# Performance work log

Hardware: AMD Instinct MI355X
Metric: run time of the kernel (lower is better)

Reference implementation:

```python
import jax, jax.numpy as jnp
import numpy as np

T, B, DIM = 64, 16, 512
H, Dh, ETA = 8, 64, 4
FD = ETA * Dh  # feature_dim = 256
EPS = 1e-6


def setup_inputs() -> dict:
    key = jax.random.key(0)
    ks = jax.random.split(key, 12)

    def w(k, o, i):
        return jax.random.normal(k, (o, i), jnp.float32) * (1.0 / np.sqrt(i).astype(np.float32))

    return {
        "inputs": jax.random.normal(ks[0], (T, B, DIM), jnp.float32),
        "terminations": jax.random.randint(ks[1], (T, B), 0, 2).astype(jnp.int32),
        "kv_state_prev": jnp.zeros((B, H, FD, Dh), jnp.float32),
        "norm_state_prev": jnp.zeros((B, H, FD), jnp.float32),
        "Wq": w(ks[2], H * Dh, DIM),
        "Wk": w(ks[3], H * Dh, DIM),
        "Wv": w(ks[4], H * Dh, DIM),
        "Wb": w(ks[5], H * Dh, DIM),
        "Wg": w(ks[6], H * Dh, DIM),
        "Wp1": w(ks[7], H * ETA, DIM),
        "Wp2": w(ks[8], H * ETA, DIM),
        "Wp3": w(ks[9], H * ETA, DIM),
        "Wo": w(ks[10], DIM, H * Dh),
        "bo": jnp.zeros((DIM,), jnp.float32),
    }


def reference(inputs, terminations, kv_state_prev, norm_state_prev,
              Wq, Wk, Wv, Wb, Wg, Wp1, Wp2, Wp3, Wo, bo):
    def proj(W, e):
        return (inputs @ W.T).reshape(T, B, H, e)

    q = proj(Wq, Dh)
    k = proj(Wk, Dh)
    v = proj(Wv, Dh)
    beta = jax.nn.sigmoid(proj(Wb, Dh))
    gamma = jax.nn.sigmoid(proj(Wg, Dh))
    p1 = proj(Wp1, ETA)
    p2 = proj(Wp2, ETA)
    p3 = proj(Wp3, ETA)

    # feature map: outer product of relu(p) [eta] and x [head_dim] -> [eta*head_dim]
    def fmap(x, p):
        return jnp.einsum('tbhe,tbhd->tbhed', jax.nn.relu(p), x).reshape(T, B, H, FD)

    phi_q = fmap(q, p2)
    psi_k = fmap(k, p1)
    # gamma map: outer product of sigmoid(p3) and sigmoid-gated gamma, values in (0,1)
    gamma_feat = jnp.einsum('tbhe,tbhd->tbhed', jax.nn.sigmoid(p3), gamma).reshape(T, B, H, FD)

    gated_v = v * beta                       # [T,B,H,Dh]
    gated_k = psi_k * gamma_feat             # [T,B,H,FD]

    term_mask = (1.0 - terminations.astype(jnp.float32))[:, :, None, None]  # [T,B,1,1]
    discount = (1.0 - gamma_feat) * term_mask  # [T,B,H,FD]

    kv_upd = jnp.einsum('tbhd,tbhD->tbhDd', gated_v, gated_k)  # [T,B,H,FD,Dh]

    def step(carry, x):
        kv, nm = carry
        d, u_kv, u_nm = x
        kv = d[..., None] * kv + u_kv
        nm = d * nm + u_nm
        return (kv, nm), (kv, nm)

    _, (kv_all, nm_all) = jax.lax.scan(step, (kv_state_prev, norm_state_prev),
                                       (discount, kv_upd, gated_k))

    attn_num = jnp.einsum('tbhDd,tbhD->tbhd', kv_all, phi_q)
    attn_den = jnp.einsum('tbhD,tbhD->tbh', phi_q, nm_all)
    attn_out = (attn_num / (attn_den[..., None] + EPS)).reshape(T, B, H * Dh)
    output = attn_out @ Wo.T + bo
    return (output, kv_all[-1], nm_all[-1])
```

## Files before the change

### kernel.cpp

```cpp
#include <hip/hip_runtime.h>


#define T_N   64
#define B_N   16
#define DIM_N 512
#define H_N   8
#define DH_N  64

#define OUT_ELEMS   524288
#define KV_ELEMS    2097152
#define PROJ_ELEMS  2719744

typedef _Float16 f16;
typedef f16   f16x8 __attribute__((ext_vector_type(8)));
typedef float f32x4 __attribute__((ext_vector_type(4)));

__device__ __forceinline__ float sigmoidf_(float x) {
    return 1.0f / (1.0f + __expf(-x));
}

__device__ __forceinline__ void gemm64_core(const float* __restrict__ A,
                                            const float* __restrict__ W,
                                            const float* __restrict__ bias,
                                            float* __restrict__ C, int N,
                                            int mb, int nb, int kBase, int kLen) {
    const int nbase = nb * 64;
    if (nbase >= N) return;

    __shared__ float As[2][16][68];
    __shared__ float Bs[2][16][68];

    const int tid = threadIdx.x;
    const int mbase = mb * 64;
    const int tx = tid & 15;
    const int ty = tid >> 4;
    const int sr = tid >> 2;
    const int sk = (tid & 3) << 2;
    const bool wok = (nbase + sr) < N;

    const float* Ap = A + (size_t)(mbase + sr) * 512 + kBase + sk;
    const float* Wp = W + (size_t)(nbase + sr) * 512 + kBase + sk;

    float4 av = *(const float4*)Ap;
    float4 wv = wok ? *(const float4*)Wp : make_float4(0.f, 0.f, 0.f, 0.f);
    As[0][sk + 0][sr] = av.x; As[0][sk + 1][sr] = av.y;
    As[0][sk + 2][sr] = av.z; As[0][sk + 3][sr] = av.w;
    Bs[0][sk + 0][sr] = wv.x; Bs[0][sk + 1][sr] = wv.y;
    Bs[0][sk + 2][sr] = wv.z; Bs[0][sk + 3][sr] = wv.w;

    float acc[4][4];
    #pragma unroll
    for (int i = 0; i < 4; ++i)
        #pragma unroll
        for (int j = 0; j < 4; ++j) acc[i][j] = 0.f;

    for (int k0 = 0; k0 < kLen; k0 += 16) {
        const int buf = (k0 >> 4) & 1;
        __syncthreads();
        const bool more = (k0 + 16) < kLen;
        if (more) {
            av = *(const float4*)(Ap + k0 + 16);
            wv = wok ? *(const float4*)(Wp + k0 + 16) : make_float4(0.f, 0.f, 0.f, 0.f);
        }
        #pragma unroll
        for (int k = 0; k < 16; ++k) {
            float4 a  = *(const float4*)&As[buf][k][ty << 2];
            float4 bq = *(const float4*)&Bs[buf][k][tx << 2];
            float ar[4] = {a.x, a.y, a.z, a.w};
            float br[4] = {bq.x, bq.y, bq.z, bq.w};
            #pragma unroll
            for (int i = 0; i < 4; ++i)
                #pragma unroll
                for (int j = 0; j < 4; ++j)
                    acc[i][j] = fmaf(ar[i], br[j], acc[i][j]);
        }
        if (more) {
            const int nbuf = buf ^ 1;
            As[nbuf][sk + 0][sr] = av.x; As[nbuf][sk + 1][sr] = av.y;
            As[nbuf][sk + 2][sr] = av.z; As[nbuf][sk + 3][sr] = av.w;
            Bs[nbuf][sk + 0][sr] = wv.x; Bs[nbuf][sk + 1][sr] = wv.y;
            Bs[nbuf][sk + 2][sr] = wv.z; Bs[nbuf][sk + 3][sr] = wv.w;
        }
    }

    #pragma unroll
    for (int i = 0; i < 4; ++i) {
        const int m = mbase + (ty << 2) + i;
        #pragma unroll
        for (int j = 0; j < 4; ++j) {
            const int n = nbase + (tx << 2) + j;
            if (n < N) {
                float v = acc[i][j];
                if (bias) v += bias[n];
                C[(size_t)m * N + n] = v;
            }
        }
    }
}

struct ProjW {
    const float* W[8];
    float*       D[8];
};

__device__ __forceinline__ void cvt_split_store(f16* __restrict__ dh,
                                                f16* __restrict__ dl,
                                                float4 v0, float4 v1) {
    float x[8] = {v0.x, v0.y, v0.z, v0.w, v1.x, v1.y, v1.z, v1.w};
    f16x8 h, lo;
    #pragma unroll
    for (int e = 0; e < 8; ++e) {
        f16 hh = (f16)x[e];
        h[e]  = hh;
        lo[e] = (f16)(x[e] - (float)hh);
    }
    *(f16x8*)dh = h;
    *(f16x8*)dl = lo;
}

__global__ __launch_bounds__(256) void proj_mfma_kernel(const float* __restrict__ X,
                                                        ProjW a) {
    const int id = blockIdx.x;
    const int z = id & 7;
    const int rem = id >> 3;
    const int mb = rem & 15;
    const int nb = rem >> 4;
    const int N = (z < 5) ? 512 : 32;
    const int nbase = nb * 64;
    if (nbase >= N) return;

    const float* __restrict__ W = a.W[z];
    float* __restrict__ C = a.D[z];
    const int mbase = mb * 64;

    __shared__ f16 AsH[2][64][40];
    __shared__ f16 AsL[2][64][40];
    __shared__ f16 BsH[2][64][40];
    __shared__ f16 BsL[2][64][40];

    const int tid = threadIdx.x;
    const int sr = tid >> 2;
    const int kq = (tid & 3) << 3;
    const bool wok = (nbase + sr) < N;
    const float* Ap = X + (size_t)(mbase + sr) * 512 + kq;
    const float* Wp = W + (size_t)(nbase + sr) * 512 + kq;

    const int l  = tid & 63;
    const int w  = tid >> 6;
    const int wr = (w >> 1) << 5;
    const int wc = (w & 1) << 5;
    const int lr = l & 15;
    const int lk = (l >> 4) << 3;

    f32x4 acc[2][2] = {};

    float4 xa0 = *(const float4*)(Ap);
    float4 xa1 = *(const float4*)(Ap + 4);
    float4 wb0 = wok ? *(const float4*)(Wp)     : make_float4(0.f, 0.f, 0.f, 0.f);
    float4 wb1 = wok ? *(const float4*)(Wp + 4) : make_float4(0.f, 0.f, 0.f, 0.f);
    cvt_split_store(&AsH[0][sr][kq], &AsL[0][sr][kq], xa0, xa1);
    cvt_split_store(&BsH[0][sr][kq], &BsL[0][sr][kq], wb0, wb1);

    for (int k0 = 0; k0 < 512; k0 += 32) {
        const int buf = (k0 >> 5) & 1;
        __syncthreads();
        const bool more = (k0 + 32) < 512;
        if (more) {
            xa0 = *(const float4*)(Ap + k0 + 32);
            xa1 = *(const float4*)(Ap + k0 + 36);
            wb0 = wok ? *(const float4*)(Wp + k0 + 32) : make_float4(0.f, 0.f, 0.f, 0.f);
            wb1 = wok ? *(const float4*)(Wp + k0 + 36) : make_float4(0.f, 0.f, 0.f, 0.f);
        }

        f16x8 aH[2], aL[2], bH[2], bL[2];
        #pragma unroll
        for (int i = 0; i < 2; ++i) {
            const int row = wr + i * 16 + lr;
            aH[i] = *(const f16x8*)&AsH[buf][row][lk];
            aL[i] = *(const f16x8*)&AsL[buf][row][lk];
        }
        #pragma unroll
        for (int j = 0; j < 2; ++j) {
            const int col = wc + j * 16 + lr;
            bH[j] = *(const f16x8*)&BsH[buf][col][lk];
            bL[j] = *(const f16x8*)&BsL[buf][col][lk];
        }

        #pragma unroll
        for (int i = 0; i < 2; ++i)
            #pragma unroll
            for (int j = 0; j < 2; ++j) {
                acc[i][j] = __builtin_amdgcn_mfma_f32_16x16x32_f16(aH[i], bH[j], acc[i][j], 0, 0, 0);
                acc[i][j] = __builtin_amdgcn_mfma_f32_16x16x32_f16(aH[i], bL[j], acc[i][j], 0, 0, 0);
                acc[i][j] = __builtin_amdgcn_mfma_f32_16x16x32_f16(aL[i], bH[j], acc[i][j], 0, 0, 0);
            }

        if (more) {
            const int nbuf = buf ^ 1;
            cvt_split_store(&AsH[nbuf][sr][kq], &AsL[nbuf][sr][kq], xa0, xa1);
            cvt_split_store(&BsH[nbuf][sr][kq], &BsL[nbuf][sr][kq], wb0, wb1);
        }
    }

    #pragma unroll
    for (int j = 0; j < 2; ++j) {
        const int n = nbase + wc + j * 16 + lr;
        if (n < N) {
            #pragma unroll
            for (int i = 0; i < 2; ++i) {
                #pragma unroll
                for (int q = 0; q < 4; ++q) {
                    const int m = mbase + wr + i * 16 + ((l >> 4) << 2) + q;
                    C[(size_t)m * N + n] = acc[i][j][q];
                }
            }
        }
    }
}

__global__ __launch_bounds__(256) void out_gemm_kernel(const float* __restrict__ A,
                                                       const float* __restrict__ W,
                                                       const float* __restrict__ bias,
                                                       float* __restrict__ C) {
    gemm64_core(A, W, bias, C, 512, blockIdx.x, blockIdx.y, 0, 512);
}

struct OutP { float* P[4]; };
__global__ __launch_bounds__(256) void out_partial_kernel(const float* __restrict__ A,
                                                          const float* __restrict__ W,
                                                          OutP p) {
    const int id = blockIdx.x;
    const int m = id & 15;
    const int n = (id >> 4) & 7;
    const int kq = id >> 7;
    gemm64_core(A, W, nullptr, p.P[kq], 512, m, n, kq * 128, 128);
}

__global__ __launch_bounds__(256) void out_reduce_kernel(
    const float* __restrict__ p0, const float* __restrict__ p1,
    const float* __restrict__ p2, const float* __restrict__ p3,
    const float* __restrict__ bias, float* __restrict__ out) {
    const int i = blockIdx.x * 256 + threadIdx.x;
    float4 a = ((const float4*)p0)[i];
    float4 b = ((const float4*)p1)[i];
    float4 c = ((const float4*)p2)[i];
    float4 d = ((const float4*)p3)[i];
    float4 bv = ((const float4*)bias)[i & 127];
    float4 r;
    r.x = a.x + b.x + c.x + d.x + bv.x;
    r.y = a.y + b.y + c.y + d.y + bv.y;
    r.z = a.z + b.z + c.z + d.z + bv.z;
    r.w = a.w + b.w + c.w + d.w + bv.w;
    ((float4*)out)[i] = r;
}

__global__ __launch_bounds__(256) void gate_kernel(
    const float* __restrict__ qb,  const float* __restrict__ kb,
    const float* __restrict__ vb,  const float* __restrict__ bb,
    const float* __restrict__ gb,  const float* __restrict__ p1b,
    const float* __restrict__ p2b, const float* __restrict__ p3b,
    const int* __restrict__ term,
    float* __restrict__ disc_g, float* __restrict__ gk_g,
    float* __restrict__ phiq_g, float* __restrict__ gv_g) {
    const int h = blockIdx.x;
    const int row = blockIdx.y;
    const int D = threadIdx.x;
    const int e = D >> 6, di = D & 63;
    const size_t base = (size_t)row * 512 + h * 64;
    const size_t pb = (size_t)row * 32 + h * 4;

    float q = qb[base + di], k = kb[base + di], g = gb[base + di];
    float p1 = p1b[pb + e], p2 = p2b[pb + e], p3 = p3b[pb + e];
    float mask = 1.0f - (float)term[row];
    float gf = sigmoidf_(p3) * sigmoidf_(g);

    const size_t o = ((size_t)row * 8 + h) * 256 + D;
    disc_g[o] = (1.0f - gf) * mask;
    gk_g[o]   = fmaxf(p1, 0.f) * k * gf;
    phiq_g[o] = fmaxf(p2, 0.f) * q;
    if (D < 64)
        gv_g[((size_t)row * 8 + h) * 64 + D] = vb[base + D] * sigmoidf_(bb[base + D]);
}

__global__ __launch_bounds__(256) void scan5_kernel(
    const float* __restrict__ disc_g, const float* __restrict__ gk_g,
    const float* __restrict__ phiq_g, const float* __restrict__ gv_g,
    float* __restrict__ vb ,
    const float* __restrict__ kv0, const float* __restrict__ nm0,
    float* __restrict__ dout) {
    const int blk = blockIdx.x;
    const int bh = blk & 127;
    const int s  = blk >> 7;
    const int b  = bh >> 3;
    const int h  = bh & 7;
    const int tid = threadIdx.x;
    const int w = tid >> 6;
    const int l = tid & 63;
    const int half = l >> 5;
    const int li = l & 31;
    const int d0 = s * 16 + w * 4 + half * 2;
    const int D0 = li << 3;

    float kv[8][2];
    float nm[8];
    {
        const float* kp = kv0 + ((size_t)bh * 256 + D0) * 64 + d0;
        #pragma unroll
        for (int j = 0; j < 8; ++j) {
            float2 r = *(const float2*)(kp + (size_t)j * 64);
            kv[j][0] = r.x; kv[j][1] = r.y;
        }
        float4 na = *(const float4*)(nm0 + (size_t)bh * 256 + D0);
        float4 nb_ = *(const float4*)(nm0 + (size_t)bh * 256 + D0 + 4);
        nm[0] = na.x; nm[1] = na.y; nm[2] = na.z; nm[3] = na.w;
        nm[4] = nb_.x; nm[5] = nb_.y; nm[6] = nb_.z; nm[7] = nb_.w;
    }

    float4 cd0, cd1, cg0, cg1, cp0, cp1; float2 cgv;
    {
        const size_t go = ((size_t)b * 8 + h) * 256 + D0;
        cd0 = *(const float4*)(disc_g + go);  cd1 = *(const float4*)(disc_g + go + 4);
        cg0 = *(const float4*)(gk_g + go);    cg1 = *(const float4*)(gk_g + go + 4);
        cp0 = *(const float4*)(phiq_g + go);  cp1 = *(const float4*)(phiq_g + go + 4);
        cgv = *(const float2*)(gv_g + ((size_t)b * 8 + h) * 64 + d0);
    }

    for (int t = 0; t < T_N; ++t) {
        const int row = t * B_N + b;
        const size_t base = (size_t)row * 512 + h * 64;

        float4 nd0 = {}, nd1 = {}, ng0 = {}, ng1 = {}, np0 = {}, np1 = {};
        float2 ngv = {};
        if (t + 1 < T_N) {
            const size_t go2 = ((size_t)(row + B_N) * 8 + h) * 256 + D0;
            nd0 = *(const float4*)(disc_g + go2); nd1 = *(const float4*)(disc_g + go2 + 4);
            ng0 = *(const float4*)(gk_g + go2);   ng1 = *(const float4*)(gk_g + go2 + 4);
            np0 = *(const float4*)(phiq_g + go2); np1 = *(const float4*)(phiq_g + go2 + 4);
            ngv = *(const float2*)(gv_g + ((size_t)(row + B_N) * 8 + h) * 64 + d0);
        }

        const float dj[8]  = {cd0.x, cd0.y, cd0.z, cd0.w, cd1.x, cd1.y, cd1.z, cd1.w};
        const float gkj[8] = {cg0.x, cg0.y, cg0.z, cg0.w, cg1.x, cg1.y, cg1.z, cg1.w};
        const float phj[8] = {cp0.x, cp0.y, cp0.z, cp0.w, cp1.x, cp1.y, cp1.z, cp1.w};

        float den = 0.f, n0 = 0.f, n1 = 0.f;
        #pragma unroll
        for (int j = 0; j < 8; ++j) {
            nm[j] = dj[j] * nm[j] + gkj[j];
            den = fmaf(phj[j], nm[j], den);
            kv[j][0] = dj[j] * kv[j][0] + gkj[j] * cgv.x; n0 = fmaf(phj[j], kv[j][0], n0);
            kv[j][1] = dj[j] * kv[j][1] + gkj[j] * cgv.y; n1 = fmaf(phj[j], kv[j][1], n1);
        }

        #pragma unroll
        for (int ofs = 1; ofs <= 16; ofs <<= 1) {
            n0  += __shfl_xor(n0, ofs);
            n1  += __shfl_xor(n1, ofs);
            den += __shfl_xor(den, ofs);
        }

        if (li == 0) {
            vb[base + d0]     = n0 / (den + 1e-6f);
            vb[base + d0 + 1] = n1 / (den + 1e-6f);
        }

        cd0 = nd0; cd1 = nd1; cg0 = ng0; cg1 = ng1; cp0 = np0; cp1 = np1; cgv = ngv;
    }

    {
        float* kp = dout + OUT_ELEMS + ((size_t)bh * 256 + D0) * 64 + d0;
        #pragma unroll
        for (int j = 0; j < 8; ++j)
            *(float2*)(kp + (size_t)j * 64) = make_float2(kv[j][0], kv[j][1]);
        if (s == 0 && w == 0 && half == 0) {
            float* np = dout + OUT_ELEMS + KV_ELEMS + (size_t)bh * 256 + D0;
            *(float4*)np       = make_float4(nm[0], nm[1], nm[2], nm[3]);
            *(float4*)(np + 4) = make_float4(nm[4], nm[5], nm[6], nm[7]);
        }
    }
}

extern "C" void kernel_launch(void* const* d_in, const int* in_sizes, int n_in,
                              void* d_out, int out_size, void* d_ws, size_t ws_size,
                              hipStream_t stream) {
    (void)in_sizes; (void)n_in; (void)out_size;

    const float* X    = (const float*)d_in[0];
    const int*   term = (const int*)  d_in[1];
    const float* kv0  = (const float*)d_in[2];
    const float* nm0  = (const float*)d_in[3];
    const float* Wo   = (const float*)d_in[12];
    const float* bo   = (const float*)d_in[13];

    float* out = (float*)d_out;

    float* qb  = (float*)d_ws;
    float* kb  = qb  + 524288;
    float* vb  = kb  + 524288;
    float* bb  = vb  + 524288;
    float* gb  = bb  + 524288;
    float* p1b = gb  + 524288;
    float* p2b = p1b + 32768;
    float* p3b = p2b + 32768;
    float* disc_g = p3b + 32768;
    float* gk_g   = disc_g + 2097152;
    float* phiq_g = gk_g   + 2097152;
    float* gv_g   = phiq_g + 2097152;
    const size_t need_bytes = (size_t)(PROJ_ELEMS + 6815744) * 4;
    const bool big = ws_size >= need_bytes;

    ProjW pa;
    pa.W[0] = (const float*)d_in[4];  pa.W[1] = (const float*)d_in[5];
    pa.W[2] = (const float*)d_in[6];  pa.W[3] = (const float*)d_in[7];
    pa.W[4] = (const float*)d_in[8];  pa.W[5] = (const float*)d_in[9];
    pa.W[6] = (const float*)d_in[10]; pa.W[7] = (const float*)d_in[11];
    pa.D[0] = qb;  pa.D[1] = kb;  pa.D[2] = vb;  pa.D[3] = bb;
    pa.D[4] = gb;  pa.D[5] = p1b; pa.D[6] = p2b; pa.D[7] = p3b;
    proj_mfma_kernel<<<1024, 256, 0, stream>>>(X, pa);

    gate_kernel<<<dim3(8, 1024), 256, 0, stream>>>(qb, kb, vb, bb, gb,
                                                   p1b, p2b, p3b, term,
                                                   disc_g, gk_g, phiq_g, gv_g);
    scan5_kernel<<<512, 256, 0, stream>>>(disc_g, gk_g, phiq_g, gv_g,
                                          vb, kv0, nm0, out);
    if (big) {
        OutP op; op.P[0] = qb; op.P[1] = kb; op.P[2] = bb; op.P[3] = gb;
        out_partial_kernel<<<512, 256, 0, stream>>>(vb, Wo, op);
        out_reduce_kernel<<<512, 256, 0, stream>>>(qb, kb, bb, gb, bo, out);
    } else {
        out_gemm_kernel<<<dim3(16, 8), 256, 0, stream>>>(vb, Wo, bo, out);
    }
}
```

Measured before the change: 182.3 us.

## Split scan across more blocks and batch shuffle reductions over eight timesteps

The scan kernel now gives each lane one value column instead of two and launches twice as many blocks, so more wavefronts share the sequential recurrence. It also defers the cross-lane shuffle reductions, doing them for eight timesteps at once instead of every step, which takes the reduction latency off the per-step critical path. The cost is that every block redundantly reloads the per-step gate vectors and recomputes the norm state. Register use also rises from the partial-sum arrays.

Result: slower. 221.0 us (+21.2%).

```diff
diff --git a/kernel.cpp b/kernel.cpp
--- a/kernel.cpp
+++ b/kernel.cpp
@@ -282,7 +282,7 @@
         gv_g[((size_t)row * 8 + h) * 64 + D] = vb[base + D] * sigmoidf_(bb[base + D]);
 }
 
-__global__ __launch_bounds__(256) void scan5_kernel(
+__global__ __launch_bounds__(256) void scan6_kernel(
     const float* __restrict__ disc_g, const float* __restrict__ gk_g,
     const float* __restrict__ phiq_g, const float* __restrict__ gv_g,
     float* __restrict__ vb ,
@@ -298,80 +298,87 @@
     const int l = tid & 63;
     const int half = l >> 5;
     const int li = l & 31;
-    const int d0 = s * 16 + w * 4 + half * 2;
+    const int d0 = s * 8 + w * 2 + half;
     const int D0 = li << 3;
 
-    float kv[8][2];
+    float kv[8];
     float nm[8];
     {
         const float* kp = kv0 + ((size_t)bh * 256 + D0) * 64 + d0;
         #pragma unroll
-        for (int j = 0; j < 8; ++j) {
-            float2 r = *(const float2*)(kp + (size_t)j * 64);
-            kv[j][0] = r.x; kv[j][1] = r.y;
-        }
-        float4 na = *(const float4*)(nm0 + (size_t)bh * 256 + D0);
+        for (int j = 0; j < 8; ++j) kv[j] = kp[(size_t)j * 64];
+        float4 na  = *(const float4*)(nm0 + (size_t)bh * 256 + D0);
         float4 nb_ = *(const float4*)(nm0 + (size_t)bh * 256 + D0 + 4);
         nm[0] = na.x; nm[1] = na.y; nm[2] = na.z; nm[3] = na.w;
         nm[4] = nb_.x; nm[5] = nb_.y; nm[6] = nb_.z; nm[7] = nb_.w;
     }
 
-    float4 cd0, cd1, cg0, cg1, cp0, cp1; float2 cgv;
+    float4 cd0, cd1, cg0, cg1, cp0, cp1; float cgv;
     {
         const size_t go = ((size_t)b * 8 + h) * 256 + D0;
         cd0 = *(const float4*)(disc_g + go);  cd1 = *(const float4*)(disc_g + go + 4);
         cg0 = *(const float4*)(gk_g + go);    cg1 = *(const float4*)(gk_g + go + 4);
         cp0 = *(const float4*)(phiq_g + go);  cp1 = *(const float4*)(phiq_g + go + 4);
-        cgv = *(const float2*)(gv_g + ((size_t)b * 8 + h) * 64 + d0);
-    }
-
-    for (int t = 0; t < T_N; ++t) {
-        const int row = t * B_N + b;
-        const size_t base = (size_t)row * 512 + h * 64;
-
-        float4 nd0 = {}, nd1 = {}, ng0 = {}, ng1 = {}, np0 = {}, np1 = {};
-        float2 ngv = {};
-        if (t + 1 < T_N) {
-            const size_t go2 = ((size_t)(row + B_N) * 8 + h) * 256 + D0;
-            nd0 = *(const float4*)(disc_g + go2); nd1 = *(const float4*)(disc_g + go2 + 4);
-            ng0 = *(const float4*)(gk_g + go2);   ng1 = *(const float4*)(gk_g + go2 + 4);
-            np0 = *(const float4*)(phiq_g + go2); np1 = *(const float4*)(phiq_g + go2 + 4);
-            ngv = *(const float2*)(gv_g + ((size_t)(row + B_N) * 8 + h) * 64 + d0);
-        }
-
-        const float dj[8]  = {cd0.x, cd0.y, cd0.z, cd0.w, cd1.x, cd1.y, cd1.z, cd1.w};
-        const float gkj[8] = {cg0.x, cg0.y, cg0.z, cg0.w, cg1.x, cg1.y, cg1.z, cg1.w};
-        const float phj[8] = {cp0.x, cp0.y, cp0.z, cp0.w, cp1.x, cp1.y, cp1.z, cp1.w};
-
-        float den = 0.f, n0 = 0.f, n1 = 0.f;
-        #pragma unroll
-        for (int j = 0; j < 8; ++j) {
-            nm[j] = dj[j] * nm[j] + gkj[j];
-            den = fmaf(phj[j], nm[j], den);
-            kv[j][0] = dj[j] * kv[j][0] + gkj[j] * cgv.x; n0 = fmaf(phj[j], kv[j][0], n0);
-            kv[j][1] = dj[j] * kv[j][1] + gkj[j] * cgv.y; n1 = fmaf(phj[j], kv[j][1], n1);
+        cgv = gv_g[((size_t)b * 8 + h) * 64 + d0];
+    }
+
+    float nP[8], dP[8];
+
+    for (int tb = 0; tb < 8; ++tb) {
+        #pragma unroll
+        for (int tt = 0; tt < 8; ++tt) {
+            const int t = tb * 8 + tt;
+            const int row = t * B_N + b;
+
+            float4 nd0 = {}, nd1 = {}, ng0 = {}, ng1 = {}, np0 = {}, np1 = {};
+            float ngv = 0.f;
+            if (t + 1 < T_N) {
+                const size_t go2 = ((size_t)(row + B_N) * 8 + h) * 256 + D0;
+                nd0 = *(const float4*)(disc_g + go2); nd1 = *(const float4*)(disc_g + go2 + 4);
+                ng0 = *(const float4*)(gk_g + go2);   ng1 = *(const float4*)(gk_g + go2 + 4);
+                np0 = *(const float4*)(phiq_g + go2); np1 = *(const float4*)(phiq_g + go2 + 4);
+                ngv = gv_g[((size_t)(row + B_N) * 8 + h) * 64 + d0];
+            }
+
+            const float dj[8]  = {cd0.x, cd0.y, cd0.z, cd0.w, cd1.x, cd1.y, cd1.z, cd1.w};
+            const float gkj[8] = {cg0.x, cg0.y, cg0.z, cg0.w, cg1.x, cg1.y, cg1.z, cg1.w};
+            const float phj[8] = {cp0.x, cp0.y, cp0.z, cp0.w, cp1.x, cp1.y, cp1.z, cp1.w};
+
+            float den = 0.f, n0 = 0.f;
+            #pragma unroll
+            for (int j = 0; j < 8; ++j) {
+                nm[j] = dj[j] * nm[j] + gkj[j];
+                den = fmaf(phj[j], nm[j], den);
+                kv[j] = dj[j] * kv[j] + gkj[j] * cgv;
+                n0 = fmaf(phj[j], kv[j], n0);
+            }
+            nP[tt] = n0; dP[tt] = den;
+
+            cd0 = nd0; cd1 = nd1; cg0 = ng0; cg1 = ng1; cp0 = np0; cp1 = np1; cgv = ngv;
         }
 
         #pragma unroll
         for (int ofs = 1; ofs <= 16; ofs <<= 1) {
-            n0  += __shfl_xor(n0, ofs);
-            n1  += __shfl_xor(n1, ofs);
-            den += __shfl_xor(den, ofs);
+            #pragma unroll
+            for (int tt = 0; tt < 8; ++tt) {
+                nP[tt] += __shfl_xor(nP[tt], ofs);
+                dP[tt] += __shfl_xor(dP[tt], ofs);
+            }
         }
 
         if (li == 0) {
-            vb[base + d0]     = n0 / (den + 1e-6f);
-            vb[base + d0 + 1] = n1 / (den + 1e-6f);
-        }
-
-        cd0 = nd0; cd1 = nd1; cg0 = ng0; cg1 = ng1; cp0 = np0; cp1 = np1; cgv = ngv;
+            #pragma unroll
+            for (int tt = 0; tt < 8; ++tt) {
+                const int row = (tb * 8 + tt) * B_N + b;
+                vb[(size_t)row * 512 + h * 64 + d0] = nP[tt] / (dP[tt] + 1e-6f);
+            }
+        }
     }
 
     {
         float* kp = dout + OUT_ELEMS + ((size_t)bh * 256 + D0) * 64 + d0;
         #pragma unroll
-        for (int j = 0; j < 8; ++j)
-            *(float2*)(kp + (size_t)j * 64) = make_float2(kv[j][0], kv[j][1]);
+        for (int j = 0; j < 8; ++j) kp[(size_t)j * 64] = kv[j];
         if (s == 0 && w == 0 && half == 0) {
             float* np = dout + OUT_ELEMS + KV_ELEMS + (size_t)bh * 256 + D0;
             *(float4*)np       = make_float4(nm[0], nm[1], nm[2], nm[3]);
@@ -421,8 +428,8 @@
     gate_kernel<<<dim3(8, 1024), 256, 0, stream>>>(qb, kb, vb, bb, gb,
                                                    p1b, p2b, p3b, term,
                                                    disc_g, gk_g, phiq_g, gv_g);
-    scan5_kernel<<<512, 256, 0, stream>>>(disc_g, gk_g, phiq_g, gv_g,
-                                          vb, kv0, nm0, out);
+    scan6_kernel<<<1024, 256, 0, stream>>>(disc_g, gk_g, phiq_g, gv_g,
+                                           vb, kv0, nm0, out);
     if (big) {
         OutP op; op.P[0] = qb; op.P[1] = kb; op.P[2] = bb; op.P[3] = gb;
         out_partial_kernel<<<512, 256, 0, stream>>>(vb, Wo, op);
```
